# Kernel tuning notes

Measured on AMD Instinct MI355X. Metric: run time of the kernel, lower is better.

Reference implementation:

```python
import jax, jax.numpy as jnp
import numpy as np

N = 16384      # nodes
E = 524288     # edges (avg degree 32)
F_IN = 128     # input features
H1 = 256       # first_gcn_dimensions
H2 = 256       # second_gcn_dimensions
D1 = 64        # first_dense_neurons
D2 = 2         # second_dense_neurons (fixed by EYE=ones(2))


def setup_inputs() -> dict:
    key = jax.random.key(0)
    ks = jax.random.split(key, 8)
    w = lambda k, shp: (jax.random.normal(k, shp, jnp.float32) * 0.05)
    return dict(
        features=jax.random.normal(ks[0], (N, F_IN), jnp.float32),
        edges=jax.random.randint(ks[1], (2, E), 0, N),
        W1=w(ks[2], (F_IN, H1)), b1=jnp.zeros((H1,), jnp.float32),
        W2=w(ks[3], (H1, H2)), b2=jnp.zeros((H2,), jnp.float32),
        fc1_w=w(ks[4], (D1, H2)), fc1_b=jnp.zeros((D1,), jnp.float32),
        fc2_w=w(ks[5], (D2, D1)), fc2_b=jnp.zeros((D2,), jnp.float32),
    )


def gcn_conv(x, W, b, src, dst, n):
    """PyG GCNConv: xW, add self-loops, symmetric D^-1/2 (A+I) D^-1/2 aggregation."""
    x = x @ W
    loops = jnp.arange(n)
    s = jnp.concatenate([src, loops])
    d = jnp.concatenate([dst, loops])
    deg = jax.ops.segment_sum(jnp.ones(s.shape, x.dtype), d, num_segments=n)
    dinv = jnp.where(deg > 0, jax.lax.rsqrt(deg), 0.0)
    msg = x[s] * (dinv[s] * dinv[d])[:, None]          # gather + scale
    return jax.ops.segment_sum(msg, d, num_segments=n) + b  # scatter-add


def reference(features, edges, W1, b1, W2, b2, fc1_w, fc1_b, fc2_w, fc2_b):
    n = features.shape[0]
    src, dst = edges[0], edges[1]
    h1 = jax.nn.relu(gcn_conv(features, W1, b1, src, dst, n))
    h2 = gcn_conv(h1, W2, b2, src, dst, n)                 # [N, H2]
    a1 = jnp.tanh(h2 @ fc1_w.T + fc1_b)                    # [N, D1]
    assignment = jax.nn.softmax(a1 @ fc2_w.T + fc2_b, axis=1)  # [N, 2]
    group_features = assignment.T @ h2                     # [2, H2]
    # to_dense_adj: dense NxN adjacency, duplicate edges accumulate
    adj = jnp.zeros((n, n), h2.dtype).at[src, dst].add(1.0)
    new_adj = assignment.T @ (adj @ assignment)            # [2, 2]
    positive = jnp.clip(group_features[0][None, :], -100.0, 100.0)
    negative = jnp.clip(group_features[1][None, :], -100.0, 100.0)
    # F.normalize(p=1, dim=1) with eps=1e-12
    denom = jnp.maximum(jnp.sum(jnp.abs(new_adj), axis=1, keepdims=True), 1e-12)
    norm_diag = jnp.diag(new_adj / denom)
    pos_penalty = jnp.mean((norm_diag - 1.0) ** 2)         # MSE vs ones(2)
    graph_embedding = jnp.mean(group_features, axis=0, keepdims=True)  # [1, H2]
    return (graph_embedding, positive, negative, pos_penalty)
```

## Files before the change

### kernel.cpp

```cpp
#include <hip/hip_runtime.h>
#include <hip/hip_bf16.h>
#include <hip/hip_fp8.h>
#include <math.h>

#define N_NODES 16384
#define N_EDGES 524288
#define F_IN 128
#define H1 256
#define H2 256
#define D1 64
#define NA_GRID 512
#define DEG_CAP 96
#define SENT 16384

typedef __attribute__((ext_vector_type(8))) short short8;
typedef __attribute__((ext_vector_type(4))) float floatx4;
typedef unsigned short ushort_t;
typedef unsigned int uint_t;
typedef unsigned char uchar_t;

__device__ inline float bf2f(ushort_t u) {
    union { uint_t i; float f; } v;
    v.i = ((uint_t)u) << 16;
    return v.f;
}
__device__ inline ushort_t f2bs(float x) {
    __hip_bfloat16 h = __float2bfloat16(x);
    return *reinterpret_cast<ushort_t*>(&h);
}
__device__ inline uint_t pack2(float lo, float hi) {
    return (uint_t)f2bs(lo) | ((uint_t)f2bs(hi) << 16);
}
__device__ inline float f8tof(uint_t b) {
    __hip_fp8_e4m3 h; h.__x = (__hip_fp8_storage_t)(b & 0xff);
    return (float)h;
}
__device__ inline uint_t ftof8(float v) {
    __hip_fp8_e4m3 h(v);
    return (uint_t)h.__x;
}

__global__ __launch_bounds__(256) void prep_fill(
    const int* __restrict__ src, const int* __restrict__ dst,
    const float* __restrict__ W1, const float* __restrict__ W2,
    const float* __restrict__ fc1_w,
    int* __restrict__ cur, ushort_t* __restrict__ col,
    ushort_t* __restrict__ W1t, ushort_t* __restrict__ W2t,
    ushort_t* __restrict__ fc1bf) {
    int b = blockIdx.x, t = threadIdx.x;
    if (b < 2048) {
        int e = b * 256 + t;
        int d = dst[e];
        int pos = atomicAdd(&cur[d], 1);
        if (pos < DEG_CAP) col[d * DEG_CAP + pos] = (ushort_t)src[e];
    } else if (b < 2176) {
        int idx = (b - 2048) * 256 + t;
        int n = idx >> 7, k = idx & 127;
        W1t[idx] = f2bs(W1[k * 256 + n]);
    } else if (b < 2432) {
        int idx = (b - 2176) * 256 + t;
        int n = idx >> 8, k = idx & 255;
        W2t[idx] = f2bs(W2[k * 256 + n]);
    } else {
        int idx = (b - 2432) * 256 + t;
        fc1bf[idx] = f2bs(fc1_w[idx]);
    }
}

__global__ __launch_bounds__(256) void scale_feat(
    const float* __restrict__ features, const int* __restrict__ cnt,
    uchar_t* __restrict__ zs8, uchar_t* __restrict__ bufY8,
    ushort_t* __restrict__ col) {
    int b = blockIdx.x, t = threadIdx.x;
    if (b == 2048) {
        uint4 z4 = {0u, 0u, 0u, 0u};
        if (t < 8)
            *(uint4*)&zs8[(size_t)SENT * 128 + t * 16] = z4;
        else if (t >= 64 && t < 80)
            *(uint4*)&bufY8[(size_t)SENT * 256 + (t - 64) * 16] = z4;
        return;
    }
    int gid = b * 256 + t;
    int node = gid >> 5;
    int hl = gid & 31;
    int deg = cnt[node];
    float d = rsqrtf((float)(deg + 1));
    float4 v = *(const float4*)&features[gid * 4];
    uint_t p = ftof8(v.x * d) | (ftof8(v.y * d) << 8) |
               (ftof8(v.z * d) << 16) | (ftof8(v.w * d) << 24);
    *(uint_t*)&zs8[gid * 4] = p;
    if (deg < DEG_CAP) {
        int pad = (16 - (deg & 15)) & 15;
        if (hl < pad) col[node * DEG_CAP + deg + hl] = (ushort_t)SENT;
    }
}

__global__ __launch_bounds__(512, 4) void fused_layer1(
    const uchar_t* __restrict__ zs8, const int* __restrict__ cnt,
    const ushort_t* __restrict__ col, const float* __restrict__ b1,
    const ushort_t* __restrict__ W1t, const ushort_t* __restrict__ W2t,
    uchar_t* __restrict__ bufY8) {
    __shared__ __align__(16) ushort_t Az[16 * 136];
    __shared__ __align__(16) ushort_t Ah[16 * 264];
    __shared__ __align__(8) uint_t scol[768];
    const int tid = threadIdx.x;
    const int lane = tid & 63;
    const int wave = tid >> 6;
    const int m = lane & 15;
    const int quad = lane >> 4;
    const int row0 = blockIdx.x * 16;
    const uint_t* colu = (const uint_t*)col;

    if (tid < 384)
        *(uint2*)&scol[tid * 2] = *(const uint2*)&colu[row0 * 48 + tid * 2];
    __syncthreads();

    {
        const int nl0 = wave * 2, nl1 = wave * 2 + 1;
        const int node0 = row0 + nl0, node1 = row0 + nl1;
        const int foff = lane * 2;
        const int deg0 = cnt[node0], deg1 = cnt[node1];
        const int nb0 = (min(deg0, DEG_CAP) + 15) >> 4;
        const int nb1 = (min(deg1, DEG_CAP) + 15) >> 4;
        const int nbm = max(nb0, nb1);
        ushort_t s0 = *(const ushort_t*)&zs8[(size_t)node0 * 128 + foff];
        ushort_t s1 = *(const ushort_t*)&zs8[(size_t)node1 * 128 + foff];
        float a00 = f8tof(s0), a01 = f8tof(s0 >> 8);
        float a10 = f8tof(s1), a11 = f8tof(s1 >> 8);
        for (int tb = 0; tb < nbm; ++tb) {
            const bool p0 = tb < nb0, p1 = tb < nb1;
            uint_t w0[8], w1[8];
            if (p0) {
                #pragma unroll
                for (int k = 0; k < 8; ++k) w0[k] = scol[nl0 * 48 + tb * 8 + k];
            }
            if (p1) {
                #pragma unroll
                for (int k = 0; k < 8; ++k) w1[k] = scol[nl1 * 48 + tb * 8 + k];
            }
            ushort_t g0[16], g1[16];
            if (p0) {
                #pragma unroll
                for (int k = 0; k < 8; ++k) {
                    int j0 = w0[k] & 0xffff, j1 = w0[k] >> 16;
                    g0[2 * k]     = *(const ushort_t*)&zs8[(size_t)j0 * 128 + foff];
                    g0[2 * k + 1] = *(const ushort_t*)&zs8[(size_t)j1 * 128 + foff];
                }
            }
            if (p1) {
                #pragma unroll
                for (int k = 0; k < 8; ++k) {
                    int j0 = w1[k] & 0xffff, j1 = w1[k] >> 16;
                    g1[2 * k]     = *(const ushort_t*)&zs8[(size_t)j0 * 128 + foff];
                    g1[2 * k + 1] = *(const ushort_t*)&zs8[(size_t)j1 * 128 + foff];
                }
            }
            if (p0) {
                #pragma unroll
                for (int q = 0; q < 16; ++q) {
                    a00 += f8tof(g0[q]); a01 += f8tof(g0[q] >> 8);
                }
            }
            if (p1) {
                #pragma unroll
                for (int q = 0; q < 16; ++q) {
                    a10 += f8tof(g1[q]); a11 += f8tof(g1[q] >> 8);
                }
            }
        }
        float dn0 = rsqrtf((float)(deg0 + 1));
        float dn1 = rsqrtf((float)(deg1 + 1));
        *(uint_t*)&Az[nl0 * 136 + foff] = pack2(a00 * dn0, a01 * dn0);
        *(uint_t*)&Az[nl1 * 136 + foff] = pack2(a10 * dn1, a11 * dn1);
    }
    __syncthreads();

    const int wcol0 = wave * 32;
    floatx4 acc[2];
    const floatx4 zero4 = {0.f, 0.f, 0.f, 0.f};
    acc[0] = zero4; acc[1] = zero4;
    #pragma unroll
    for (int k0 = 0; k0 < 128; k0 += 32) {
        short8 a = *(const short8*)&Az[m * 136 + k0 + quad * 8];
        #pragma unroll
        for (int j = 0; j < 2; ++j) {
            short8 bb = *(const short8*)
                &W1t[(size_t)(wcol0 + j * 16 + m) * 128 + k0 + quad * 8];
            acc[j] = __builtin_amdgcn_mfma_f32_16x16x32_bf16(a, bb, acc[j], 0, 0, 0);
        }
    }
    #pragma unroll
    for (int j = 0; j < 2; ++j) {
        int cg = wcol0 + j * 16 + m;
        float bv = b1[cg];
        #pragma unroll
        for (int r = 0; r < 4; ++r) {
            float v = fmaxf(acc[j][r] + bv, 0.0f);
            Ah[(quad * 4 + r) * 264 + cg] = f2bs(v);
        }
    }
    __syncthreads();

    acc[0] = zero4; acc[1] = zero4;
    #pragma unroll
    for (int k0 = 0; k0 < 256; k0 += 32) {
        short8 a = *(const short8*)&Ah[m * 264 + k0 + quad * 8];
        #pragma unroll
        for (int j = 0; j < 2; ++j) {
            short8 bb = *(const short8*)
                &W2t[(size_t)(wcol0 + j * 16 + m) * 256 + k0 + quad * 8];
            acc[j] = __builtin_amdgcn_mfma_f32_16x16x32_bf16(a, bb, acc[j], 0, 0, 0);
        }
    }
    float rs4[4];
    #pragma unroll
    for (int r = 0; r < 4; ++r)
        rs4[r] = rsqrtf((float)(cnt[row0 + quad * 4 + r] + 1));
    #pragma unroll
    for (int j = 0; j < 2; ++j) {
        int cg = wcol0 + j * 16 + m;
        #pragma unroll
        for (int r = 0; r < 4; ++r)
            bufY8[(size_t)(row0 + quad * 4 + r) * 256 + cg] =
                (uchar_t)ftof8(acc[j][r] * rs4[r]);
    }
}

__global__ __launch_bounds__(512, 4) void fused_assign(
    const uchar_t* __restrict__ bufY8, const int* __restrict__ cnt,
    const ushort_t* __restrict__ col, const float* __restrict__ b2,
    const ushort_t* __restrict__ fc1bf, const float* __restrict__ fc1_b,
    const float* __restrict__ fc2_w, const float* __restrict__ fc2_b,
    float* __restrict__ assignp, float* __restrict__ gfr) {
    __shared__ __align__(16) ushort_t Ah[16 * 264];
    __shared__ __align__(8) uint_t scol[768];
    __shared__ float sha[16][65];
    __shared__ float sas0[16], sas1[16];
    const int tid = threadIdx.x;
    const int lane = tid & 63;
    const int wave = tid >> 6;
    const int m = lane & 15;
    const int quad = lane >> 4;
    const int row0 = blockIdx.x * 16;
    const uint_t* colu = (const uint_t*)col;

    if (tid < 384)
        *(uint2*)&scol[tid * 2] = *(const uint2*)&colu[row0 * 48 + tid * 2];
    __syncthreads();

    {
        const int nl0 = wave * 2, nl1 = wave * 2 + 1;
        const int node0 = row0 + nl0, node1 = row0 + nl1;
        const int foff = lane * 4;
        const int deg0 = cnt[node0], deg1 = cnt[node1];
        const int nb0 = (min(deg0, DEG_CAP) + 15) >> 4;
        const int nb1 = (min(deg1, DEG_CAP) + 15) >> 4;
        const int nbm = max(nb0, nb1);
        uint_t sv0 = *(const uint_t*)&bufY8[(size_t)node0 * 256 + foff];
        uint_t sv1 = *(const uint_t*)&bufY8[(size_t)node1 * 256 + foff];
        float a00 = f8tof(sv0),       a01 = f8tof(sv0 >> 8);
        float a02 = f8tof(sv0 >> 16), a03 = f8tof(sv0 >> 24);
        float a10 = f8tof(sv1),       a11 = f8tof(sv1 >> 8);
        float a12 = f8tof(sv1 >> 16), a13 = f8tof(sv1 >> 24);
        for (int tb = 0; tb < nbm; ++tb) {
            const bool p0 = tb < nb0, p1 = tb < nb1;
            uint_t w0[8], w1[8];
            if (p0) {
                #pragma unroll
                for (int k = 0; k < 8; ++k) w0[k] = scol[nl0 * 48 + tb * 8 + k];
            }
            if (p1) {
                #pragma unroll
                for (int k = 0; k < 8; ++k) w1[k] = scol[nl1 * 48 + tb * 8 + k];
            }
            uint_t g0[16], g1[16];
            if (p0) {
                #pragma unroll
                for (int k = 0; k < 8; ++k) {
                    int j0 = w0[k] & 0xffff, j1 = w0[k] >> 16;
                    g0[2 * k]     = *(const uint_t*)&bufY8[(size_t)j0 * 256 + foff];
                    g0[2 * k + 1] = *(const uint_t*)&bufY8[(size_t)j1 * 256 + foff];
                }
            }
            if (p1) {
                #pragma unroll
                for (int k = 0; k < 8; ++k) {
                    int j0 = w1[k] & 0xffff, j1 = w1[k] >> 16;
                    g1[2 * k]     = *(const uint_t*)&bufY8[(size_t)j0 * 256 + foff];
                    g1[2 * k + 1] = *(const uint_t*)&bufY8[(size_t)j1 * 256 + foff];
                }
            }
            if (p0) {
                #pragma unroll
                for (int q = 0; q < 16; ++q) {
                    a00 += f8tof(g0[q]);       a01 += f8tof(g0[q] >> 8);
                    a02 += f8tof(g0[q] >> 16); a03 += f8tof(g0[q] >> 24);
                }
            }
            if (p1) {
                #pragma unroll
                for (int q = 0; q < 16; ++q) {
                    a10 += f8tof(g1[q]);       a11 += f8tof(g1[q] >> 8);
                    a12 += f8tof(g1[q] >> 16); a13 += f8tof(g1[q] >> 24);
                }
            }
        }
        float di0 = rsqrtf((float)(deg0 + 1));
        float di1 = rsqrtf((float)(deg1 + 1));
        float4 bv = *(const float4*)&b2[foff];
        uint2 pk;
        pk.x = pack2(a00 * di0 + bv.x, a01 * di0 + bv.y);
        pk.y = pack2(a02 * di0 + bv.z, a03 * di0 + bv.w);
        *(uint2*)&Ah[nl0 * 264 + foff] = pk;
        pk.x = pack2(a10 * di1 + bv.x, a11 * di1 + bv.y);
        pk.y = pack2(a12 * di1 + bv.z, a13 * di1 + bv.w);
        *(uint2*)&Ah[nl1 * 264 + foff] = pk;
    }
    __syncthreads();

    if (wave < 4) {
        floatx4 acc = {0.f, 0.f, 0.f, 0.f};
        #pragma unroll
        for (int k0 = 0; k0 < 256; k0 += 32) {
            short8 a = *(const short8*)&Ah[m * 264 + k0 + quad * 8];
            short8 bb = *(const short8*)
                &fc1bf[(size_t)(wave * 16 + m) * 256 + k0 + quad * 8];
            acc = __builtin_amdgcn_mfma_f32_16x16x32_bf16(a, bb, acc, 0, 0, 0);
        }
        int cg = wave * 16 + m;
        float bv = fc1_b[cg];
        #pragma unroll
        for (int r = 0; r < 4; ++r)
            sha[quad * 4 + r][cg] = tanhf(acc[r] + bv);
    }
    __syncthreads();

    if (tid < 16) {
        float p0 = fc2_b[0], p1 = fc2_b[1];
        #pragma unroll 8
        for (int t = 0; t < 64; ++t) {
            float a = sha[tid][t];
            p0 += a * fc2_w[t];
            p1 += a * fc2_w[64 + t];
        }
        float mx = fmaxf(p0, p1);
        float e0 = expf(p0 - mx), e1 = expf(p1 - mx);
        float inv = 1.0f / (e0 + e1);
        assignp[row0 + tid] = e0 * inv;
        sas0[tid] = e0 * inv; sas1[tid] = e1 * inv;
    }
    __syncthreads();

    {
        const int f = tid & 255;
        const int which = tid >> 8;
        const float* sv = which ? sas1 : sas0;
        float acc = 0.f;
        #pragma unroll
        for (int i = 0; i < 16; ++i)
            acc += sv[i] * bf2f(Ah[i * 264 + f]);
        float* gfc = gfr + (blockIdx.x & 3) * 512;
        atomicAdd(&gfc[which * 256 + f], acc);
    }
}

__global__ __launch_bounds__(256) void newadj_fin(
    const int* __restrict__ src, const int* __restrict__ dst,
    const float* __restrict__ assignp, float* __restrict__ napart,
    int* __restrict__ cntt, const float* __restrict__ gfr,
    float* __restrict__ out) {
    __shared__ float red[4][3];
    __shared__ int sticket;
    const int tid = threadIdx.x;
    const int b = blockIdx.x;
    const int lane = tid & 63;
    const int wave = tid >> 6;

    float ss = 0.f, sd = 0.f, ssd = 0.f;
    {
        int g = (b * 256 + tid) * 4;
        int4 sv = *(const int4*)&src[g];
        int4 dv = *(const int4*)&dst[g];
        float s0 = assignp[sv.x], s1 = assignp[sv.y];
        float s2 = assignp[sv.z], s3 = assignp[sv.w];
        float d0 = assignp[dv.x], d1 = assignp[dv.y];
        float d2 = assignp[dv.z], d3 = assignp[dv.w];
        ss = s0 + s1 + s2 + s3;
        sd = d0 + d1 + d2 + d3;
        ssd = s0 * d0 + s1 * d1 + s2 * d2 + s3 * d3;
    }
    #pragma unroll
    for (int off = 32; off; off >>= 1) {
        ss += __shfl_down(ss, off);
        sd += __shfl_down(sd, off);
        ssd += __shfl_down(ssd, off);
    }
    if (lane == 0) {
        red[wave][0] = ssd; red[wave][1] = ss; red[wave][2] = sd;
    }
    __syncthreads();
    if (tid < 3) {
        float v = red[0][tid] + red[1][tid] + red[2][tid] + red[3][tid];
        __hip_atomic_store(&napart[b * 4 + tid], v, __ATOMIC_RELEASE,
                           __HIP_MEMORY_SCOPE_AGENT);
    }
    __syncthreads();
    if (tid == 0)
        sticket = __hip_atomic_fetch_add(cntt, 1, __ATOMIC_ACQ_REL,
                                         __HIP_MEMORY_SCOPE_AGENT);
    __syncthreads();
    if (sticket != NA_GRID - 1) return;

    float acc = 0.f;
    if (wave < 3) {
        for (int i = lane; i < NA_GRID; i += 64)
            acc += __hip_atomic_load(&napart[i * 4 + wave], __ATOMIC_RELAXED,
                                     __HIP_MEMORY_SCOPE_AGENT);
    }
    #pragma unroll
    for (int off = 32; off; off >>= 1) acc += __shfl_down(acc, off);
    __shared__ float na[3];
    if (lane == 0 && wave < 3) na[wave] = acc;
    __syncthreads();
    float g0 = gfr[tid] + gfr[512 + tid] + gfr[1024 + tid] + gfr[1536 + tid];
    float g1 = gfr[256 + tid] + gfr[768 + tid] + gfr[1280 + tid] + gfr[1792 + tid];
    out[tid] = 0.5f * (g0 + g1);
    out[256 + tid] = fminf(fmaxf(g0, -100.f), 100.f);
    out[512 + tid] = fminf(fmaxf(g1, -100.f), 100.f);
    if (tid == 0) {
        float Ssd = na[0], Ss = na[1], Sd = na[2];
        float n00 = Ssd;
        float n01 = Ss - Ssd;
        float n10 = Sd - Ssd;
        float n11 = (float)N_EDGES - Ss - Sd + Ssd;
        float den0 = fmaxf(fabsf(n00) + fabsf(n01), 1e-12f);
        float den1 = fmaxf(fabsf(n10) + fabsf(n11), 1e-12f);
        float x0 = n00 / den0 - 1.0f;
        float x1 = n11 / den1 - 1.0f;
        out[768] = 0.5f * (x0 * x0 + x1 * x1);
    }
}


extern "C" void kernel_launch(void* const* d_in, const int* in_sizes, int n_in,
                              void* d_out, int out_size, void* d_ws, size_t ws_size,
                              hipStream_t stream) {
    const float* features = (const float*)d_in[0];
    const int* edges = (const int*)d_in[1];
    const int* src = edges;
    const int* dst = edges + N_EDGES;
    const float* W1 = (const float*)d_in[2];
    const float* b1 = (const float*)d_in[3];
    const float* W2 = (const float*)d_in[4];
    const float* b2 = (const float*)d_in[5];
    const float* fc1_w = (const float*)d_in[6];
    const float* fc1_b = (const float*)d_in[7];
    const float* fc2_w = (const float*)d_in[8];
    const float* fc2_b = (const float*)d_in[9];
    float* out = (float*)d_out;

    char* ws = (char*)d_ws;
    auto carve = [&](size_t bytes) {
        void* q = (void*)ws;
        ws += (bytes + 255) & ~(size_t)255;
        return q;
    };
    int* cur = (int*)carve(N_NODES * 4);
    float* gfr = (float*)carve(4 * 512 * 4);
    int* cnt_na = (int*)carve(256);
    ushort_t* col = (ushort_t*)carve((size_t)N_NODES * DEG_CAP * 2);
    float* assignp = (float*)carve(N_NODES * 4);
    float* napart = (float*)carve(NA_GRID * 4 * 4);
    ushort_t* fc1bf = (ushort_t*)carve(64 * 256 * 2);
    uchar_t* zs8 = (uchar_t*)carve((size_t)(N_NODES + 1) * F_IN);
    ushort_t* W1t = (ushort_t*)carve(256 * 128 * 2);
    ushort_t* W2t = (ushort_t*)carve(256 * 256 * 2);
    uchar_t* bufY8 = (uchar_t*)carve((size_t)(N_NODES + 1) * 256);

    hipMemsetAsync(cur, 0, N_NODES * 4 + 4 * 512 * 4 + 256, stream);

    prep_fill<<<2496, 256, 0, stream>>>(src, dst, W1, W2, fc1_w,
                                        cur, col, W1t, W2t, fc1bf);
    scale_feat<<<2049, 256, 0, stream>>>(features, cur, zs8, bufY8, col);
    fused_layer1<<<N_NODES / 16, 512, 0, stream>>>(
        zs8, cur, col, b1, W1t, W2t, bufY8);
    fused_assign<<<N_NODES / 16, 512, 0, stream>>>(
        bufY8, cur, col, b2, fc1bf, fc1_b, fc2_w, fc2_b, assignp, gfr);
    newadj_fin<<<NA_GRID, 256, 0, stream>>>(src, dst, assignp, napart,
                                            cnt_na, gfr, out);
}
```

Measured before the change: 187.9 us.

## Reassociate second GCN aggregation through fc1 projection and edge-level scatter

Instead of aggregating the 256-wide second-layer features over neighbours, the change projects the pre-aggregation features through fc1 inside fused_layer1 to a 64-wide fp8 buffer. The neighbour gather then runs on 64 columns, with the bias folded into a precomputed constant. Group features are no longer formed by aggregating h2. They come from per-node weights built by an edge-level atomic scatter (q0/q1), followed by a dense weighted sum over the un-aggregated features, plus a bias term scaled by the summed assignment. This cuts the heavy 256-wide neighbour gather to a 64-wide one. In exchange it adds an extra kernel, per-edge float atomics and different fp8/bf16 rounding points.

Result: slower. 252.2 us (+34.2%).

```diff
diff --git a/kernel.cpp b/kernel.cpp
--- a/kernel.cpp
+++ b/kernel.cpp
@@ -6,12 +6,9 @@
 #define N_NODES 16384
 #define N_EDGES 524288
 #define F_IN 128
-#define H1 256
-#define H2 256
-#define D1 64
-#define NA_GRID 512
 #define DEG_CAP 96
 #define SENT 16384
+#define GF_GRID 256
 
 typedef __attribute__((ext_vector_type(8))) short short8;
 typedef __attribute__((ext_vector_type(4))) float floatx4;
@@ -69,15 +66,28 @@
 
 __global__ __launch_bounds__(256) void scale_feat(
     const float* __restrict__ features, const int* __restrict__ cnt,
-    uchar_t* __restrict__ zs8, uchar_t* __restrict__ bufY8,
-    ushort_t* __restrict__ col) {
+    uchar_t* __restrict__ zs8, uchar_t* __restrict__ ts8,
+    ushort_t* __restrict__ col, const float* __restrict__ fc1_w,
+    const float* __restrict__ b2, const float* __restrict__ fc1_b,
+    float* __restrict__ c1f) {
     int b = blockIdx.x, t = threadIdx.x;
     if (b == 2048) {
-        uint4 z4 = {0u, 0u, 0u, 0u};
-        if (t < 8)
-            *(uint4*)&zs8[(size_t)SENT * 128 + t * 16] = z4;
-        else if (t >= 64 && t < 80)
-            *(uint4*)&bufY8[(size_t)SENT * 256 + (t - 64) * 16] = z4;
+        if (t < 64) {
+            float acc = fc1_b[t];
+            #pragma unroll 4
+            for (int k = 0; k < 256; k += 4) {
+                float4 w = *(const float4*)&fc1_w[t * 256 + k];
+                float4 bb = *(const float4*)&b2[k];
+                acc += w.x * bb.x + w.y * bb.y + w.z * bb.z + w.w * bb.w;
+            }
+            c1f[t] = acc;
+        } else if (t < 72) {
+            uint4 z4 = {0u, 0u, 0u, 0u};
+            *(uint4*)&zs8[(size_t)SENT * 128 + (t - 64) * 16] = z4;
+        } else if (t < 76) {
+            uint4 z4 = {0u, 0u, 0u, 0u};
+            *(uint4*)&ts8[(size_t)SENT * 64 + (t - 72) * 16] = z4;
+        }
         return;
     }
     int gid = b * 256 + t;
@@ -99,7 +109,8 @@
     const uchar_t* __restrict__ zs8, const int* __restrict__ cnt,
     const ushort_t* __restrict__ col, const float* __restrict__ b1,
     const ushort_t* __restrict__ W1t, const ushort_t* __restrict__ W2t,
-    uchar_t* __restrict__ bufY8) {
+    const ushort_t* __restrict__ fc1bf,
+    uchar_t* __restrict__ bufY8, uchar_t* __restrict__ ts8) {
     __shared__ __align__(16) ushort_t Az[16 * 136];
     __shared__ __align__(16) ushort_t Ah[16 * 264];
     __shared__ __align__(8) uint_t scol[768];
@@ -114,7 +125,6 @@
     if (tid < 384)
         *(uint2*)&scol[tid * 2] = *(const uint2*)&colu[row0 * 48 + tid * 2];
     __syncthreads();
-
     {
         const int nl0 = wave * 2, nl1 = wave * 2 + 1;
         const int node0 = row0 + nl0, node1 = row0 + nl1;
@@ -174,7 +184,6 @@
         *(uint_t*)&Az[nl1 * 136 + foff] = pack2(a10 * dn1, a11 * dn1);
     }
     __syncthreads();
-
     const int wcol0 = wave * 32;
     floatx4 acc[2];
     const floatx4 zero4 = {0.f, 0.f, 0.f, 0.f};
@@ -191,16 +200,15 @@
     }
     #pragma unroll
     for (int j = 0; j < 2; ++j) {
-        int cg = wcol0 + j * 16 + m;
-        float bv = b1[cg];
+        int cg_ = wcol0 + j * 16 + m;
+        float bv = b1[cg_];
         #pragma unroll
         for (int r = 0; r < 4; ++r) {
             float v = fmaxf(acc[j][r] + bv, 0.0f);
-            Ah[(quad * 4 + r) * 264 + cg] = f2bs(v);
-        }
-    }
-    __syncthreads();
-
+            Ah[(quad * 4 + r) * 264 + cg_] = f2bs(v);
+        }
+    }
+    __syncthreads();
     acc[0] = zero4; acc[1] = zero4;
     #pragma unroll
     for (int k0 = 0; k0 < 256; k0 += 32) {
@@ -216,178 +224,128 @@
     #pragma unroll
     for (int r = 0; r < 4; ++r)
         rs4[r] = rsqrtf((float)(cnt[row0 + quad * 4 + r] + 1));
+    __syncthreads();
     #pragma unroll
     for (int j = 0; j < 2; ++j) {
-        int cg = wcol0 + j * 16 + m;
-        #pragma unroll
-        for (int r = 0; r < 4; ++r)
-            bufY8[(size_t)(row0 + quad * 4 + r) * 256 + cg] =
-                (uchar_t)ftof8(acc[j][r] * rs4[r]);
-    }
-}
-
-__global__ __launch_bounds__(512, 4) void fused_assign(
-    const uchar_t* __restrict__ bufY8, const int* __restrict__ cnt,
-    const ushort_t* __restrict__ col, const float* __restrict__ b2,
-    const ushort_t* __restrict__ fc1bf, const float* __restrict__ fc1_b,
-    const float* __restrict__ fc2_w, const float* __restrict__ fc2_b,
-    float* __restrict__ assignp, float* __restrict__ gfr) {
-    __shared__ __align__(16) ushort_t Ah[16 * 264];
-    __shared__ __align__(8) uint_t scol[768];
-    __shared__ float sha[16][65];
-    __shared__ float sas0[16], sas1[16];
-    const int tid = threadIdx.x;
-    const int lane = tid & 63;
-    const int wave = tid >> 6;
-    const int m = lane & 15;
-    const int quad = lane >> 4;
-    const int row0 = blockIdx.x * 16;
-    const uint_t* colu = (const uint_t*)col;
-
-    if (tid < 384)
-        *(uint2*)&scol[tid * 2] = *(const uint2*)&colu[row0 * 48 + tid * 2];
-    __syncthreads();
-
-    {
-        const int nl0 = wave * 2, nl1 = wave * 2 + 1;
-        const int node0 = row0 + nl0, node1 = row0 + nl1;
-        const int foff = lane * 4;
-        const int deg0 = cnt[node0], deg1 = cnt[node1];
-        const int nb0 = (min(deg0, DEG_CAP) + 15) >> 4;
-        const int nb1 = (min(deg1, DEG_CAP) + 15) >> 4;
-        const int nbm = max(nb0, nb1);
-        uint_t sv0 = *(const uint_t*)&bufY8[(size_t)node0 * 256 + foff];
-        uint_t sv1 = *(const uint_t*)&bufY8[(size_t)node1 * 256 + foff];
-        float a00 = f8tof(sv0),       a01 = f8tof(sv0 >> 8);
-        float a02 = f8tof(sv0 >> 16), a03 = f8tof(sv0 >> 24);
-        float a10 = f8tof(sv1),       a11 = f8tof(sv1 >> 8);
-        float a12 = f8tof(sv1 >> 16), a13 = f8tof(sv1 >> 24);
-        for (int tb = 0; tb < nbm; ++tb) {
-            const bool p0 = tb < nb0, p1 = tb < nb1;
-            uint_t w0[8], w1[8];
-            if (p0) {
-                #pragma unroll
-                for (int k = 0; k < 8; ++k) w0[k] = scol[nl0 * 48 + tb * 8 + k];
-            }
-            if (p1) {
-                #pragma unroll
-                for (int k = 0; k < 8; ++k) w1[k] = scol[nl1 * 48 + tb * 8 + k];
-            }
-            uint_t g0[16], g1[16];
-            if (p0) {
-                #pragma unroll
-                for (int k = 0; k < 8; ++k) {
-                    int j0 = w0[k] & 0xffff, j1 = w0[k] >> 16;
-                    g0[2 * k]     = *(const uint_t*)&bufY8[(size_t)j0 * 256 + foff];
-                    g0[2 * k + 1] = *(const uint_t*)&bufY8[(size_t)j1 * 256 + foff];
-                }
-            }
-            if (p1) {
-                #pragma unroll
-                for (int k = 0; k < 8; ++k) {
-                    int j0 = w1[k] & 0xffff, j1 = w1[k] >> 16;
-                    g1[2 * k]     = *(const uint_t*)&bufY8[(size_t)j0 * 256 + foff];
-                    g1[2 * k + 1] = *(const uint_t*)&bufY8[(size_t)j1 * 256 + foff];
-                }
-            }
-            if (p0) {
-                #pragma unroll
-                for (int q = 0; q < 16; ++q) {
-                    a00 += f8tof(g0[q]);       a01 += f8tof(g0[q] >> 8);
-                    a02 += f8tof(g0[q] >> 16); a03 += f8tof(g0[q] >> 24);
-                }
-            }
-            if (p1) {
-                #pragma unroll
-                for (int q = 0; q < 16; ++q) {
-                    a10 += f8tof(g1[q]);       a11 += f8tof(g1[q] >> 8);
-                    a12 += f8tof(g1[q] >> 16); a13 += f8tof(g1[q] >> 24);
-                }
-            }
-        }
-        float di0 = rsqrtf((float)(deg0 + 1));
-        float di1 = rsqrtf((float)(deg1 + 1));
-        float4 bv = *(const float4*)&b2[foff];
-        uint2 pk;
-        pk.x = pack2(a00 * di0 + bv.x, a01 * di0 + bv.y);
-        pk.y = pack2(a02 * di0 + bv.z, a03 * di0 + bv.w);
-        *(uint2*)&Ah[nl0 * 264 + foff] = pk;
-        pk.x = pack2(a10 * di1 + bv.x, a11 * di1 + bv.y);
-        pk.y = pack2(a12 * di1 + bv.z, a13 * di1 + bv.w);
-        *(uint2*)&Ah[nl1 * 264 + foff] = pk;
-    }
-    __syncthreads();
-
+        int cg_ = wcol0 + j * 16 + m;
+        #pragma unroll
+        for (int r = 0; r < 4; ++r) {
+            float ys = acc[j][r] * rs4[r];
+            bufY8[(size_t)(row0 + quad * 4 + r) * 256 + cg_] = (uchar_t)ftof8(ys);
+            Ah[(quad * 4 + r) * 264 + cg_] = f2bs(ys);
+        }
+    }
+    __syncthreads();
     if (wave < 4) {
-        floatx4 acc = {0.f, 0.f, 0.f, 0.f};
+        floatx4 at = zero4;
         #pragma unroll
         for (int k0 = 0; k0 < 256; k0 += 32) {
             short8 a = *(const short8*)&Ah[m * 264 + k0 + quad * 8];
             short8 bb = *(const short8*)
                 &fc1bf[(size_t)(wave * 16 + m) * 256 + k0 + quad * 8];
-            acc = __builtin_amdgcn_mfma_f32_16x16x32_bf16(a, bb, acc, 0, 0, 0);
-        }
-        int cg = wave * 16 + m;
-        float bv = fc1_b[cg];
+            at = __builtin_amdgcn_mfma_f32_16x16x32_bf16(a, bb, at, 0, 0, 0);
+        }
+        int cg_ = wave * 16 + m;
         #pragma unroll
         for (int r = 0; r < 4; ++r)
-            sha[quad * 4 + r][cg] = tanhf(acc[r] + bv);
-    }
-    __syncthreads();
-
-    if (tid < 16) {
-        float p0 = fc2_b[0], p1 = fc2_b[1];
-        #pragma unroll 8
-        for (int t = 0; t < 64; ++t) {
-            float a = sha[tid][t];
-            p0 += a * fc2_w[t];
-            p1 += a * fc2_w[64 + t];
-        }
-        float mx = fmaxf(p0, p1);
-        float e0 = expf(p0 - mx), e1 = expf(p1 - mx);
-        float inv = 1.0f / (e0 + e1);
-        assignp[row0 + tid] = e0 * inv;
-        sas0[tid] = e0 * inv; sas1[tid] = e1 * inv;
-    }
-    __syncthreads();
-
-    {
-        const int f = tid & 255;
-        const int which = tid >> 8;
-        const float* sv = which ? sas1 : sas0;
-        float acc = 0.f;
-        #pragma unroll
-        for (int i = 0; i < 16; ++i)
-            acc += sv[i] * bf2f(Ah[i * 264 + f]);
-        float* gfc = gfr + (blockIdx.x & 3) * 512;
-        atomicAdd(&gfc[which * 256 + f], acc);
-    }
-}
-
-__global__ __launch_bounds__(256) void newadj_fin(
+            ts8[(size_t)(row0 + quad * 4 + r) * 64 + cg_] = (uchar_t)ftof8(at[r]);
+    }
+}
+
+__global__ __launch_bounds__(512, 4) void assign2(
+    const uchar_t* __restrict__ ts8, const int* __restrict__ cnt,
+    const ushort_t* __restrict__ col, const float* __restrict__ c1f,
+    const float* __restrict__ fc2_w, const float* __restrict__ fc2_b,
+    float* __restrict__ packf, float* __restrict__ P0acc) {
+    __shared__ __align__(8) uint_t scol[768];
+    __shared__ float sP[16];
+    const int tid = threadIdx.x;
+    const int lane = tid & 63;
+    const int wave = tid >> 6;
+    const int half = lane >> 5;
+    const int il = lane & 31;
+    const int row0 = blockIdx.x * 16;
+    const uint_t* colu = (const uint_t*)col;
+
+    if (tid < 384)
+        *(uint2*)&scol[tid * 2] = *(const uint2*)&colu[row0 * 48 + tid * 2];
+    __syncthreads();
+
+    const int nl = wave * 2 + half;
+    const int node = row0 + nl;
+    const int foff = il * 2;
+    const int deg = cnt[node];
+    const int nb = (min(deg, DEG_CAP) + 15) >> 4;
+    ushort_t sv = *(const ushort_t*)&ts8[(size_t)node * 64 + foff];
+    float a0 = f8tof(sv), a1 = f8tof(sv >> 8);
+    for (int tb = 0; tb < nb; ++tb) {
+        uint_t w[8];
+        #pragma unroll
+        for (int k = 0; k < 8; ++k) w[k] = scol[nl * 48 + tb * 8 + k];
+        ushort_t g[16];
+        #pragma unroll
+        for (int k = 0; k < 8; ++k) {
+            int j0 = w[k] & 0xffff, j1 = w[k] >> 16;
+            g[2 * k]     = *(const ushort_t*)&ts8[(size_t)j0 * 64 + foff];
+            g[2 * k + 1] = *(const ushort_t*)&ts8[(size_t)j1 * 64 + foff];
+        }
+        #pragma unroll
+        for (int q = 0; q < 16; ++q) {
+            a0 += f8tof(g[q]); a1 += f8tof(g[q] >> 8);
+        }
+    }
+    float dinv = rsqrtf((float)(deg + 1));
+    float t0 = tanhf(dinv * a0 + c1f[foff]);
+    float t1 = tanhf(dinv * a1 + c1f[foff + 1]);
+    float part0 = t0 * fc2_w[foff] + t1 * fc2_w[foff + 1];
+    float part1 = t0 * fc2_w[64 + foff] + t1 * fc2_w[64 + foff + 1];
+    #pragma unroll
+    for (int mask = 1; mask < 32; mask <<= 1) {
+        part0 += __shfl_xor(part0, mask);
+        part1 += __shfl_xor(part1, mask);
+    }
+    if (il == 0) {
+        float l0 = fc2_b[0] + part0, l1 = fc2_b[1] + part1;
+        float mx = fmaxf(l0, l1);
+        float e0 = expf(l0 - mx), e1 = expf(l1 - mx);
+        float p0v = e0 / (e0 + e1);
+        float4 pk;
+        pk.x = p0v; pk.y = p0v * dinv; pk.z = dinv; pk.w = 0.f;
+        *(float4*)&packf[node * 4] = pk;
+        sP[nl] = p0v;
+    }
+    __syncthreads();
+    if (tid == 0) {
+        float s = 0.f;
+        #pragma unroll
+        for (int i = 0; i < 16; ++i) s += sP[i];
+        atomicAdd(P0acc, s);
+    }
+}
+
+__global__ __launch_bounds__(256) void edge_q(
     const int* __restrict__ src, const int* __restrict__ dst,
-    const float* __restrict__ assignp, float* __restrict__ napart,
-    int* __restrict__ cntt, const float* __restrict__ gfr,
-    float* __restrict__ out) {
+    const float* __restrict__ packf, float* __restrict__ q0,
+    float* __restrict__ q1, float* __restrict__ napart) {
     __shared__ float red[4][3];
-    __shared__ int sticket;
     const int tid = threadIdx.x;
     const int b = blockIdx.x;
     const int lane = tid & 63;
     const int wave = tid >> 6;
 
     float ss = 0.f, sd = 0.f, ssd = 0.f;
-    {
-        int g = (b * 256 + tid) * 4;
-        int4 sv = *(const int4*)&src[g];
-        int4 dv = *(const int4*)&dst[g];
-        float s0 = assignp[sv.x], s1 = assignp[sv.y];
-        float s2 = assignp[sv.z], s3 = assignp[sv.w];
-        float d0 = assignp[dv.x], d1 = assignp[dv.y];
-        float d2 = assignp[dv.z], d3 = assignp[dv.w];
-        ss = s0 + s1 + s2 + s3;
-        sd = d0 + d1 + d2 + d3;
-        ssd = s0 * d0 + s1 * d1 + s2 * d2 + s3 * d3;
+    int g = (b * 256 + tid) * 4;
+    int4 sv = *(const int4*)&src[g];
+    int4 dv = *(const int4*)&dst[g];
+    #pragma unroll
+    for (int e = 0; e < 4; ++e) {
+        int s = (e == 0) ? sv.x : (e == 1) ? sv.y : (e == 2) ? sv.z : sv.w;
+        int d = (e == 0) ? dv.x : (e == 1) ? dv.y : (e == 2) ? dv.z : dv.w;
+        float ps = packf[s * 4];
+        float4 pd = *(const float4*)&packf[d * 4];
+        ss += ps; sd += pd.x; ssd += ps * pd.x;
+        atomicAdd(&q0[s], pd.y);
+        atomicAdd(&q1[s], pd.z - pd.y);
     }
     #pragma unroll
     for (int off = 32; off; off >>= 1) {
@@ -404,16 +362,60 @@
         __hip_atomic_store(&napart[b * 4 + tid], v, __ATOMIC_RELEASE,
                            __HIP_MEMORY_SCOPE_AGENT);
     }
+}
+
+__global__ __launch_bounds__(256) void gf_fin(
+    const uchar_t* __restrict__ bufY8, const float* __restrict__ packf,
+    const float* __restrict__ q0, const float* __restrict__ q1,
+    const float* __restrict__ napart, float* __restrict__ gfr,
+    const float* __restrict__ P0acc, const float* __restrict__ b2,
+    int* __restrict__ cntt, float* __restrict__ out) {
+    __shared__ float sred[4][512];
+    __shared__ int sticket;
+    const int tid = threadIdx.x;
+    const int lane = tid & 63;
+    const int wave = tid >> 6;
+    const int nb0 = blockIdx.x * 64;
+
+    float f0[4] = {0.f, 0.f, 0.f, 0.f};
+    float f1[4] = {0.f, 0.f, 0.f, 0.f};
+    for (int n = wave; n < 64; n += 4) {
+        int node = nb0 + n;
+        float4 pk = *(const float4*)&packf[node * 4];
+        float w0 = pk.y + q0[node];
+        float w1 = (pk.z - pk.y) + q1[node];
+        uint_t v = *(const uint_t*)&bufY8[(size_t)node * 256 + lane * 4];
+        #pragma unroll
+        for (int i = 0; i < 4; ++i) {
+            float x = f8tof(v >> (8 * i));
+            f0[i] += w0 * x;
+            f1[i] += w1 * x;
+        }
+    }
+    #pragma unroll
+    for (int i = 0; i < 4; ++i) {
+        sred[wave][lane * 4 + i] = f0[i];
+        sred[wave][256 + lane * 4 + i] = f1[i];
+    }
+    __syncthreads();
+    float* gfc = gfr + (blockIdx.x & 3) * 512;
+    {
+        float v0 = sred[0][tid] + sred[1][tid] + sred[2][tid] + sred[3][tid];
+        float v1 = sred[0][256 + tid] + sred[1][256 + tid] +
+                   sred[2][256 + tid] + sred[3][256 + tid];
+        atomicAdd(&gfc[tid], v0);
+        atomicAdd(&gfc[256 + tid], v1);
+    }
     __syncthreads();
     if (tid == 0)
         sticket = __hip_atomic_fetch_add(cntt, 1, __ATOMIC_ACQ_REL,
                                          __HIP_MEMORY_SCOPE_AGENT);
     __syncthreads();
-    if (sticket != NA_GRID - 1) return;
+    if (sticket != GF_GRID - 1) return;
 
     float acc = 0.f;
     if (wave < 3) {
-        for (int i = lane; i < NA_GRID; i += 64)
+        for (int i = lane; i < 512; i += 64)
             acc += __hip_atomic_load(&napart[i * 4 + wave], __ATOMIC_RELAXED,
                                      __HIP_MEMORY_SCOPE_AGENT);
     }
@@ -422,11 +424,25 @@
     __shared__ float na[3];
     if (lane == 0 && wave < 3) na[wave] = acc;
     __syncthreads();
-    float g0 = gfr[tid] + gfr[512 + tid] + gfr[1024 + tid] + gfr[1536 + tid];
-    float g1 = gfr[256 + tid] + gfr[768 + tid] + gfr[1280 + tid] + gfr[1792 + tid];
-    out[tid] = 0.5f * (g0 + g1);
-    out[256 + tid] = fminf(fmaxf(g0, -100.f), 100.f);
-    out[512 + tid] = fminf(fmaxf(g1, -100.f), 100.f);
+    float P0 = __hip_atomic_load(P0acc, __ATOMIC_RELAXED,
+                                 __HIP_MEMORY_SCOPE_AGENT);
+    float P1 = (float)N_NODES - P0;
+    {
+        float g0 = 0.f, g1 = 0.f;
+        #pragma unroll
+        for (int k = 0; k < 4; ++k) {
+            g0 += __hip_atomic_load(&gfr[k * 512 + tid], __ATOMIC_RELAXED,
+                                    __HIP_MEMORY_SCOPE_AGENT);
+            g1 += __hip_atomic_load(&gfr[k * 512 + 256 + tid], __ATOMIC_RELAXED,
+                                    __HIP_MEMORY_SCOPE_AGENT);
+        }
+        float bv = b2[tid];
+        g0 += P0 * bv;
+        g1 += P1 * bv;
+        out[tid] = 0.5f * (g0 + g1);
+        out[256 + tid] = fminf(fmaxf(g0, -100.f), 100.f);
+        out[512 + tid] = fminf(fmaxf(g1, -100.f), 100.f);
+    }
     if (tid == 0) {
         float Ssd = na[0], Ss = na[1], Sd = na[2];
         float n00 = Ssd;
@@ -468,24 +484,33 @@
     int* cur = (int*)carve(N_NODES * 4);
     float* gfr = (float*)carve(4 * 512 * 4);
     int* cnt_na = (int*)carve(256);
+    float* q0 = (float*)carve(N_NODES * 4);
+    float* q1 = (float*)carve(N_NODES * 4);
+    float* P0acc = (float*)carve(256);
+    const size_t MEMSET_BYTES = 65536 + 8192 + 256 + 65536 + 65536 + 256;
+
     ushort_t* col = (ushort_t*)carve((size_t)N_NODES * DEG_CAP * 2);
-    float* assignp = (float*)carve(N_NODES * 4);
-    float* napart = (float*)carve(NA_GRID * 4 * 4);
+    float* packf = (float*)carve((size_t)N_NODES * 4 * 4);
+    float* napart = (float*)carve(512 * 4 * 4);
     ushort_t* fc1bf = (ushort_t*)carve(64 * 256 * 2);
+    float* c1f = (float*)carve(64 * 4);
     uchar_t* zs8 = (uchar_t*)carve((size_t)(N_NODES + 1) * F_IN);
     ushort_t* W1t = (ushort_t*)carve(256 * 128 * 2);
     ushort_t* W2t = (ushort_t*)carve(256 * 256 * 2);
     uchar_t* bufY8 = (uchar_t*)carve((size_t)(N_NODES + 1) * 256);
-
-    hipMemsetAsync(cur, 0, N_NODES * 4 + 4 * 512 * 4 + 256, stream);
+    uchar_t* ts8 = (uchar_t*)carve((size_t)(N_NODES + 1) * 64);
+
+    hipMemsetAsync(cur, 0, MEMSET_BYTES, stream);
 
     prep_fill<<<2496, 256, 0, stream>>>(src, dst, W1, W2, fc1_w,
                                         cur, col, W1t, W2t, fc1bf);
-    scale_feat<<<2049, 256, 0, stream>>>(features, cur, zs8, bufY8, col);
+    scale_feat<<<2049, 256, 0, stream>>>(features, cur, zs8, ts8, col,
+                                         fc1_w, b2, fc1_b, c1f);
     fused_layer1<<<N_NODES / 16, 512, 0, stream>>>(
-        zs8, cur, col, b1, W1t, W2t, bufY8);
-    fused_assign<<<N_NODES / 16, 512, 0, stream>>>(
-        bufY8, cur, col, b2, fc1bf, fc1_b, fc2_w, fc2_b, assignp, gfr);
-    newadj_fin<<<NA_GRID, 256, 0, stream>>>(src, dst, assignp, napart,
-                                            cnt_na, gfr, out);
-}
+        zs8, cur, col, b1, W1t, W2t, fc1bf, bufY8, ts8);
+    assign2<<<N_NODES / 16, 512, 0, stream>>>(
+        ts8, cur, col, c1f, fc2_w, fc2_b, packf, P0acc);
+    edge_q<<<512, 256, 0, stream>>>(src, dst, packf, q0, q1, napart);
+    gf_fin<<<GF_GRID, 256, 0, stream>>>(bufY8, packf, q0, q1, napart, gfr,
+                                        P0acc, b2, cnt_na, out);
+}
```
